# Optimization experiments

Hardware: AMD Instinct MI355X
Metric: run time of the kernel (lower is better)

## Reference

```python
import jax, jax.numpy as jnp
from jax import lax
import numpy as np

# Dims
B_, CIN, COUT, T = 2, 64, 128, 8192
K, NM, N, DCONV, EXP = 5, 2, 16, 4, 2   # kernel, n_mamba, d_state, d_conv, expand
DI = EXP * COUT                          # d_inner = 256
DTR = (COUT + 15) // 16                  # dt_rank = 8
M = NM * 2                               # mamba instances (fwd+bwd per block)


def setup_inputs() -> dict:
    key = jax.random.key(0)
    ks = jax.random.split(key, 8)
    r = lambda k, s, sc=0.02: (jax.random.normal(k, s) * sc).astype(jnp.float32)
    return {
        "x": jax.random.normal(ks[0], (B_, CIN, T), dtype=jnp.float32),
        "conv_w": r(ks[1], (COUT, CIN, K), 0.05),
        "conv_b": jnp.zeros((COUT,), jnp.float32),
        "gn_g": jnp.ones((COUT,), jnp.float32),
        "gn_b": jnp.zeros((COUT,), jnp.float32),
        "prelu_a": jnp.full((1,), 0.25, jnp.float32),
        "ln_g": jnp.ones((NM, COUT), jnp.float32),
        "ln_b": jnp.zeros((NM, COUT), jnp.float32),
        "W_in": r(ks[2], (M, 2 * DI, COUT)),
        "conv1d_w": r(ks[3], (M, DI, 1, DCONV), 0.1),
        "conv1d_b": jnp.zeros((M, DI), jnp.float32),
        "W_xproj": r(ks[4], (M, DTR + 2 * N, DI)),
        "W_dt": r(ks[5], (M, DI, DTR), 0.1),
        "b_dt": jnp.full((M, DI), -4.0, jnp.float32),
        "A_log": jnp.broadcast_to(jnp.log(jnp.arange(1, N + 1, dtype=jnp.float32)), (M, DI, N)).copy(),
        "D_param": jnp.ones((M, DI), jnp.float32),
        "W_out": r(ks[6], (M, COUT, DI)),
    }


def _silu(x):
    return x * jax.nn.sigmoid(x)


def _layernorm(x, g, b, eps=1e-5):
    mu = x.mean(-1, keepdims=True)
    v = ((x - mu) ** 2).mean(-1, keepdims=True)
    return (x - mu) * lax.rsqrt(v + eps) * g + b


def _mamba(h, Wi, cw, cb, Wx, Wd, bd, Alog, Dp, Wo):
    # h: [B, L, d_model] -> [B, L, d_model]. Standard Mamba (S6) block.
    Bb, L, _ = h.shape
    xz = jnp.einsum('bld,ed->ble', h, Wi)               # [B,L,2*DI]
    xp, z = jnp.split(xz, 2, axis=-1)
    xc = jnp.transpose(xp, (0, 2, 1))                   # [B,DI,L]
    xc = lax.conv_general_dilated(xc, cw, (1,), [(DCONV - 1, 0)],
                                  feature_group_count=DI,
                                  dimension_numbers=('NCH', 'OIH', 'NCH')) + cb[None, :, None]
    u = _silu(jnp.transpose(xc, (0, 2, 1)))             # [B,L,DI]
    xdbl = jnp.einsum('bld,ed->ble', u, Wx)             # [B,L,DTR+2N]
    dt, Bm, Cm = jnp.split(xdbl, [DTR, DTR + N], axis=-1)
    delta = jax.nn.softplus(jnp.einsum('blr,dr->bld', dt, Wd) + bd)  # [B,L,DI]
    A = -jnp.exp(Alog)                                  # [DI,N]
    dA = jnp.exp(delta[..., None] * A)                  # [B,L,DI,N]
    dBu = (delta * u)[..., None] * Bm[:, :, None, :]    # [B,L,DI,N]

    def step(hc, inp):
        a, b, c = inp
        hc = a * hc + b                                  # [B,DI,N]
        return hc, jnp.einsum('bdn,bn->bd', hc, c)

    h0 = jnp.zeros((Bb, DI, N), dtype=h.dtype)
    _, ys = lax.scan(step, h0, (jnp.moveaxis(dA, 1, 0), jnp.moveaxis(dBu, 1, 0), jnp.moveaxis(Cm, 1, 0)))
    y = jnp.moveaxis(ys, 0, 1) + u * Dp                 # [B,L,DI]
    y = y * _silu(z)
    return jnp.einsum('ble,de->bld', y, Wo)


def reference(x, conv_w, conv_b, gn_g, gn_b, prelu_a, ln_g, ln_b, W_in,
              conv1d_w, conv1d_b, W_xproj, W_dt, b_dt, A_log, D_param, W_out):
    # Conv1d stride 2, padding K//2: [B,CIN,T] -> [B,COUT,T//2]
    h = lax.conv_general_dilated(x, conv_w, (2,), [(K // 2, K // 2)],
                                 dimension_numbers=('NCH', 'OIH', 'NCH')) + conv_b[None, :, None]
    # GroupNorm(1, COUT): normalize jointly over (C, T)
    mu = h.mean((1, 2), keepdims=True)
    v = ((h - mu) ** 2).mean((1, 2), keepdims=True)
    h = (h - mu) * lax.rsqrt(v + 1e-5) * gn_g[None, :, None] + gn_b[None, :, None]
    h = jnp.where(h >= 0, h, prelu_a[0] * h)            # PReLU (shared scalar)
    h = jnp.transpose(h, (0, 2, 1))                     # [B, L, C]
    for i in range(NM):
        hn = _layernorm(h, ln_g[i], ln_b[i])
        f, bw = 2 * i, 2 * i + 1
        yf = _mamba(hn, W_in[f], conv1d_w[f], conv1d_b[f], W_xproj[f], W_dt[f], b_dt[f], A_log[f], D_param[f], W_out[f])
        hb = jnp.flip(hn, axis=1)
        yb = jnp.flip(_mamba(hb, W_in[bw], conv1d_w[bw], conv1d_b[bw], W_xproj[bw], W_dt[bw], b_dt[bw], A_log[bw], D_param[bw], W_out[bw]), axis=1)
        h = h + yf + yb                                  # bidirectional residual
    return jnp.transpose(h, (0, 2, 1))                   # [B, COUT, T//2]
```

## Files before the change

kernel.cpp:

```cpp
#include <hip/hip_runtime.h>
#include <hip/hip_bf16.h>
#include <math.h>

constexpr int B2   = 2;
constexpr int CIN  = 64;
constexpr int COUT = 128;
constexpr int T    = 8192;
constexpr int L    = 4096;
constexpr int DI   = 256;
constexpr int NST  = 16;
constexpr int DTR  = 8;
constexpr int Q    = 32;
constexpr int NC   = 128;
constexpr int TOK  = B2 * L;

typedef __attribute__((ext_vector_type(8))) short bf16x8s;
typedef __attribute__((ext_vector_type(4))) float f32x4;

__device__ __forceinline__ float sigmoidf_(float x) { return 1.f / (1.f + __expf(-x)); }
__device__ __forceinline__ unsigned short f2bf(float f) {
    unsigned int u = __float_as_uint(f);
    unsigned int r = (u + 0x7FFFu + ((u >> 16) & 1u)) >> 16;
    return (unsigned short)r;
}
__device__ __forceinline__ float bf2f(unsigned short s) {
    return __uint_as_float((unsigned int)s << 16);
}

__global__ __launch_bounds__(256) void prep_all_kernel(
    const float* __restrict__ W_in, const float* __restrict__ W_out,
    const float* __restrict__ cw,
    unsigned short* __restrict__ Winb, unsigned short* __restrict__ Woutb,
    unsigned short* __restrict__ Wrb, float* __restrict__ stats) {
    int idx = blockIdx.x * 256 + threadIdx.x;
    if (blockIdx.x == 0 && threadIdx.x < 4) stats[threadIdx.x] = 0.f;
    if (idx < 262144) {
        Winb[idx] = f2bf(W_in[idx]);
    } else if (idx < 393216) {
        int i = idx - 262144; Woutb[i] = f2bf(W_out[i]);
    } else if (idx < 434176) {
        int i = idx - 393216;
        int co = i / 320, r = i % 320;
        int kp = r >> 6, ci = r & 63;
        Wrb[i] = f2bf(cw[co * 320 + ci * 5 + kp]);
    }
}

__global__ __launch_bounds__(256) void xpose_kernel(
    const float* __restrict__ x, unsigned short* __restrict__ xTb) {
    __shared__ float tile[64][65];
    int b = blockIdx.y, tb = blockIdx.x * 64, tid = threadIdx.x;
    #pragma unroll
    for (int i = 0; i < 16; ++i) {
        int idx = i * 256 + tid; int ci = idx >> 6, tt = idx & 63;
        tile[ci][tt] = x[((size_t)b * CIN + ci) * T + tb + tt];
    }
    __syncthreads();
    #pragma unroll
    for (int i = 0; i < 16; ++i) {
        int idx = i * 256 + tid; int tt = idx >> 6, ci = idx & 63;
        xTb[((size_t)b * T + tb + tt) * 64 + ci] = f2bf(tile[ci][tt]);
    }
}

__global__ __launch_bounds__(256) void conv_mfma_kernel(
    const unsigned short* __restrict__ xTb, const unsigned short* __restrict__ Wrb,
    const float* __restrict__ cb, float* __restrict__ h, float* __restrict__ stats) {
    const int tid = threadIdx.x;
    const int w = tid >> 6, lane = tid & 63, q = lane >> 4, c = lane & 15;
    const int t0g = blockIdx.x * 64;
    const int t0  = t0g + w * 16;
    const int ct0 = blockIdx.y * 64;
    const int b   = t0g >> 12;
    const int l   = (t0 + c) & (L - 1);
    f32x4 acc[4] = {};
    for (int kc = 0; kc < 320; kc += 32) {
        int kp  = kc >> 6;
        int ci0 = (kc & 63) + q * 8;
        int p = 2 * l + kp - 2;
        bf16x8s a = {};
        if (p >= 0 && p < T)
            a = *(const bf16x8s*)&xTb[((size_t)b * T + p) * 64 + ci0];
        #pragma unroll
        for (int i = 0; i < 4; ++i) {
            bf16x8s bb = *(const bf16x8s*)&Wrb[(size_t)(ct0 + i * 16 + c) * 320 + kc + q * 8];
            acc[i] = __builtin_amdgcn_mfma_f32_16x16x32_bf16(a, bb, acc[i], 0, 0, 0);
        }
    }
    float s = 0.f, ss = 0.f;
    #pragma unroll
    for (int i = 0; i < 4; ++i) {
        int cout = ct0 + i * 16 + c;
        float bias = cb[cout];
        #pragma unroll
        for (int r = 0; r < 4; ++r) {
            int tok = t0 + q * 4 + r;
            float v = acc[i][r] + bias;
            h[(size_t)tok * COUT + cout] = v;
            s += v; ss += v * v;
        }
    }
    #pragma unroll
    for (int off = 32; off; off >>= 1) {
        s  += __shfl_down(s,  off, 64);
        ss += __shfl_down(ss, off, 64);
    }
    if (lane == 0) {
        atomicAdd(&stats[b * 2 + 0], s);
        atomicAdd(&stats[b * 2 + 1], ss);
    }
}

__global__ __launch_bounds__(256) void gn_prelu_kernel(
    float* __restrict__ h, const float* __restrict__ gn_g,
    const float* __restrict__ gn_b, const float* __restrict__ prelu_a,
    const float* __restrict__ stats) {
    int i = blockIdx.x * 256 + threadIdx.x;
    size_t base = (size_t)i * 4;
    int b = (base >= (size_t)L * COUT) ? 1 : 0;
    const float n = (float)(L * COUT);
    float mu   = stats[b * 2 + 0] / n;
    float var  = stats[b * 2 + 1] / n - mu * mu;
    float rstd = rsqrtf(var + 1e-5f);
    float a = prelu_a[0];
    float4 v = *(const float4*)&h[base];
    int c = (int)(base % COUT);
    float4 g  = *(const float4*)&gn_g[c];
    float4 bb = *(const float4*)&gn_b[c];
    v.x = (v.x - mu) * rstd * g.x + bb.x; v.x = v.x >= 0.f ? v.x : a * v.x;
    v.y = (v.y - mu) * rstd * g.y + bb.y; v.y = v.y >= 0.f ? v.y : a * v.y;
    v.z = (v.z - mu) * rstd * g.z + bb.z; v.z = v.z >= 0.f ? v.z : a * v.z;
    v.w = (v.w - mu) * rstd * g.w + bb.w; v.w = v.w >= 0.f ? v.w : a * v.w;
    *(float4*)&h[base] = v;
}

__global__ __launch_bounds__(256) void ln_kernel(
    const float* __restrict__ h, unsigned short* __restrict__ hnb,
    const float* __restrict__ g, const float* __restrict__ bta) {
    int wave = threadIdx.x >> 6, lane = threadIdx.x & 63;
    int t = blockIdx.x * 4 + wave;
    const float* row = h + (size_t)t * COUT;
    float2 v = *(const float2*)&row[lane * 2];
    float s = v.x + v.y, ss = v.x * v.x + v.y * v.y;
    #pragma unroll
    for (int off = 32; off; off >>= 1) {
        s  += __shfl_xor(s,  off, 64);
        ss += __shfl_xor(ss, off, 64);
    }
    float mu = s * (1.f / 128.f);
    float var = ss * (1.f / 128.f) - mu * mu;
    float rstd = rsqrtf(var + 1e-5f);
    float2 gg = *(const float2*)&g[lane * 2];
    float2 bb = *(const float2*)&bta[lane * 2];
    ushort2 o;
    o.x = f2bf((v.x - mu) * rstd * gg.x + bb.x);
    o.y = f2bf((v.y - mu) * rstd * gg.y + bb.y);
    *(ushort2*)&hnb[(size_t)t * COUT + lane * 2] = o;
}

__global__ __launch_bounds__(256) void inproj_mfma_kernel(
    const unsigned short* __restrict__ hnb, const unsigned short* __restrict__ Winb,
    float* __restrict__ xp0, unsigned short* __restrict__ zb0,
    float* __restrict__ xp1, unsigned short* __restrict__ zb1, int layer) {
    const int tid = threadIdx.x;
    const int w = tid >> 6, lane = tid & 63, q = lane >> 4, c = lane & 15;
    const int t0 = blockIdx.x * 64 + w * 16;
    const int nBase = blockIdx.y * 64;
    const int inst = nBase >> 9;
    const int e0 = nBase & 511;
    const unsigned short* Wb = Winb + (size_t)(layer * 2 + inst) * 512 * 128;
    f32x4 acc[4] = {};
    for (int kc = 0; kc < 128; kc += 32) {
        bf16x8s a = *(const bf16x8s*)&hnb[(size_t)(t0 + c) * 128 + kc + q * 8];
        #pragma unroll
        for (int i = 0; i < 4; ++i) {
            bf16x8s bb = *(const bf16x8s*)&Wb[(size_t)(e0 + i * 16 + c) * 128 + kc + q * 8];
            acc[i] = __builtin_amdgcn_mfma_f32_16x16x32_bf16(a, bb, acc[i], 0, 0, 0);
        }
    }
    #pragma unroll
    for (int i = 0; i < 4; ++i) {
        int e = e0 + i * 16 + c;
        bool isz = (e >= 256);
        int eo = e & 255;
        #pragma unroll
        for (int r = 0; r < 4; ++r) {
            int tok = t0 + q * 4 + r;
            float v = acc[i][r];
            if (isz) {
                float sv = v * sigmoidf_(v);
                (inst ? zb1 : zb0)[(size_t)tok * DI + eo] = f2bf(sv);
            } else {
                (inst ? xp1 : xp0)[(size_t)tok * DI + eo] = v;
            }
        }
    }
}

__global__ __launch_bounds__(256) void dwconv_kernel(
    const float* __restrict__ xp0, const float* __restrict__ xp1,
    const float* __restrict__ cw, const float* __restrict__ cbias,
    float* __restrict__ u0, float* __restrict__ u1, int layer) {
    int flat = blockIdx.x * 256 + threadIdx.x;
    int dq   = flat & 63;
    int l    = (flat >> 6) & (L - 1);
    int b    = (flat >> 18) & 1;
    int inst = flat >> 19;
    const float* xp = inst ? xp1 : xp0;
    float* u = inst ? u1 : u0;
    int m = layer * 2 + inst;
    int d0 = dq * 4;
    float4 w0 = *(const float4*)&cw[(size_t)(m * DI + d0 + 0) * 4];
    float4 w1 = *(const float4*)&cw[(size_t)(m * DI + d0 + 1) * 4];
    float4 w2 = *(const float4*)&cw[(size_t)(m * DI + d0 + 2) * 4];
    float4 w3 = *(const float4*)&cw[(size_t)(m * DI + d0 + 3) * 4];
    float4 acc = *(const float4*)&cbias[m * DI + d0];
    size_t base = ((size_t)b * L) * DI + d0;
    if (inst == 0) {
        if (l >= 3) { float4 v = *(const float4*)&xp[base + (size_t)(l - 3) * DI];
            acc.x = fmaf(w0.x, v.x, acc.x); acc.y = fmaf(w1.x, v.y, acc.y);
            acc.z = fmaf(w2.x, v.z, acc.z); acc.w = fmaf(w3.x, v.w, acc.w); }
        if (l >= 2) { float4 v = *(const float4*)&xp[base + (size_t)(l - 2) * DI];
            acc.x = fmaf(w0.y, v.x, acc.x); acc.y = fmaf(w1.y, v.y, acc.y);
            acc.z = fmaf(w2.y, v.z, acc.z); acc.w = fmaf(w3.y, v.w, acc.w); }
        if (l >= 1) { float4 v = *(const float4*)&xp[base + (size_t)(l - 1) * DI];
            acc.x = fmaf(w0.z, v.x, acc.x); acc.y = fmaf(w1.z, v.y, acc.y);
            acc.z = fmaf(w2.z, v.z, acc.z); acc.w = fmaf(w3.z, v.w, acc.w); }
        { float4 v = *(const float4*)&xp[base + (size_t)l * DI];
            acc.x = fmaf(w0.w, v.x, acc.x); acc.y = fmaf(w1.w, v.y, acc.y);
            acc.z = fmaf(w2.w, v.z, acc.z); acc.w = fmaf(w3.w, v.w, acc.w); }
    } else {
        { float4 v = *(const float4*)&xp[base + (size_t)l * DI];
            acc.x = fmaf(w0.w, v.x, acc.x); acc.y = fmaf(w1.w, v.y, acc.y);
            acc.z = fmaf(w2.w, v.z, acc.z); acc.w = fmaf(w3.w, v.w, acc.w); }
        if (l + 1 < L) { float4 v = *(const float4*)&xp[base + (size_t)(l + 1) * DI];
            acc.x = fmaf(w0.z, v.x, acc.x); acc.y = fmaf(w1.z, v.y, acc.y);
            acc.z = fmaf(w2.z, v.z, acc.z); acc.w = fmaf(w3.z, v.w, acc.w); }
        if (l + 2 < L) { float4 v = *(const float4*)&xp[base + (size_t)(l + 2) * DI];
            acc.x = fmaf(w0.y, v.x, acc.x); acc.y = fmaf(w1.y, v.y, acc.y);
            acc.z = fmaf(w2.y, v.z, acc.z); acc.w = fmaf(w3.y, v.w, acc.w); }
        if (l + 3 < L) { float4 v = *(const float4*)&xp[base + (size_t)(l + 3) * DI];
            acc.x = fmaf(w0.x, v.x, acc.x); acc.y = fmaf(w1.x, v.y, acc.y);
            acc.z = fmaf(w2.x, v.z, acc.z); acc.w = fmaf(w3.x, v.w, acc.w); }
    }
    acc.x *= sigmoidf_(acc.x); acc.y *= sigmoidf_(acc.y);
    acc.z *= sigmoidf_(acc.z); acc.w *= sigmoidf_(acc.w);
    *(float4*)&u[base + (size_t)l * DI] = acc;
}

__global__ __launch_bounds__(256) void xproj_kernel(
    const float* __restrict__ u0, const float* __restrict__ u1,
    const float* __restrict__ Wx, const float* __restrict__ Wdt,
    const float* __restrict__ bdt,
    float* __restrict__ dl0, float* __restrict__ dl1,
    float* __restrict__ Bm0, float* __restrict__ Bm1,
    float* __restrict__ Cm0, float* __restrict__ Cm1, int layer) {
    __shared__ float Ws[40 * 132];
    __shared__ float As[128 * 33];
    __shared__ float xd[32 * 9];
    const int tid   = threadIdx.x;
    const int tBase = blockIdx.x * 32;
    const int inst  = blockIdx.y;
    const int m     = layer * 2 + inst;
    const float* u  = inst ? u1 : u0;
    const float* Wm = Wx + (size_t)m * 40 * 256;
    const int t  = tid & 31;
    const int eq = tid >> 5;
    float acc[5] = {};
    for (int kc = 0; kc < 256; kc += 128) {
        __syncthreads();
        #pragma unroll
        for (int i = 0; i < 5; ++i) {
            int idx = i * 256 + tid;
            int e = idx >> 5, kq = idx & 31;
            float4 w4 = *(const float4*)&Wm[(size_t)e * 256 + kc + kq * 4];
            float* dstw = &Ws[e * 132 + kq * 4];
            dstw[0] = w4.x; dstw[1] = w4.y; dstw[2] = w4.z; dstw[3] = w4.w;
        }
        #pragma unroll
        for (int i = 0; i < 4; ++i) {
            int flat = i * 256 + tid;
            int tt = flat >> 5, kq = flat & 31;
            float4 v = *(const float4*)&u[(size_t)(tBase + tt) * DI + kc + kq * 4];
            As[(kq * 4 + 0) * 33 + tt] = v.x;
            As[(kq * 4 + 1) * 33 + tt] = v.y;
            As[(kq * 4 + 2) * 33 + tt] = v.z;
            As[(kq * 4 + 3) * 33 + tt] = v.w;
        }
        __syncthreads();
        #pragma unroll 4
        for (int kk = 0; kk < 128; ++kk) {
            float a = As[kk * 33 + t];
            acc[0] = fmaf(a, Ws[(eq     ) * 132 + kk], acc[0]);
            acc[1] = fmaf(a, Ws[(eq +  8) * 132 + kk], acc[1]);
            acc[2] = fmaf(a, Ws[(eq + 16) * 132 + kk], acc[2]);
            acc[3] = fmaf(a, Ws[(eq + 24) * 132 + kk], acc[3]);
            acc[4] = fmaf(a, Ws[(eq + 32) * 132 + kk], acc[4]);
        }
    }
    {
        int tok = tBase + t;
        float* Bm = inst ? Bm1 : Bm0;
        float* Cm = inst ? Cm1 : Cm0;
        xd[t * 9 + eq] = acc[0];
        Bm[(size_t)tok * NST + eq]     = acc[1];
        Bm[(size_t)tok * NST + 8 + eq] = acc[2];
        Cm[(size_t)tok * NST + eq]     = acc[3];
        Cm[(size_t)tok * NST + 8 + eq] = acc[4];
    }
    __syncthreads();
    {
        int d = tid;
        float wr[8];
        #pragma unroll
        for (int r = 0; r < 8; ++r) wr[r] = Wdt[((size_t)m * DI + d) * DTR + r];
        float bb = bdt[m * DI + d];
        float* dl = inst ? dl1 : dl0;
        #pragma unroll 4
        for (int tt = 0; tt < 32; ++tt) {
            float a2 = bb;
            #pragma unroll
            for (int r = 0; r < 8; ++r) a2 = fmaf(xd[tt * 9 + r], wr[r], a2);
            float sp = fmaxf(a2, 0.f) + __logf(1.f + __expf(-fabsf(a2)));
            dl[(size_t)(tBase + tt) * DI + d] = sp;
        }
    }
}

__global__ __launch_bounds__(256) void scan1_kernel(
    const float* __restrict__ dl0, const float* __restrict__ dl1,
    const float* __restrict__ u0,  const float* __restrict__ u1,
    const float* __restrict__ Bm0, const float* __restrict__ Bm1,
    const float* __restrict__ A_log,
    float* __restrict__ hend, float* __restrict__ dsumb, int layer) {
    const int tid = threadIdx.x;
    const int nq = tid & 3, dlane = tid >> 2;
    const int chunk = blockIdx.x & (NC - 1), dtile = blockIdx.x >> 7;
    const int b = blockIdx.y, inst = blockIdx.z;
    const int m = layer * 2 + inst, dir = inst;
    const int d = dtile * 64 + dlane;
    const float* dl = inst ? dl1 : dl0;
    const float* u  = inst ? u1  : u0;
    const float* Bm = inst ? Bm1 : Bm0;
    float4 av = *(const float4*)&A_log[((size_t)m * DI + d) * NST + nq * 4];
    const float a0 = -expf(av.x), a1 = -expf(av.y), a2 = -expf(av.z), a3 = -expf(av.w);
    const int s0 = chunk * Q;
    const int l0 = dir ? (L - 1 - s0) : s0;
    const int stp = dir ? -1 : 1;
    long iDU = ((long)(b * L + l0)) * DI + d;
    int  iB  = ((b * L + l0) << 4) + nq * 4;
    const long sDU = (long)stp * DI;
    const int  sB  = stp * NST;
    float h0 = 0.f, h1 = 0.f, h2 = 0.f, h3 = 0.f, dsum = 0.f;
    #pragma unroll 4
    for (int t = 0; t < Q; ++t) {
        float dlt = dl[iDU], uu = u[iDU];
        float4 bm = *(const float4*)&Bm[iB];
        float du = dlt * uu;
        h0 = fmaf(__expf(dlt * a0), h0, du * bm.x);
        h1 = fmaf(__expf(dlt * a1), h1, du * bm.y);
        h2 = fmaf(__expf(dlt * a2), h2, du * bm.z);
        h3 = fmaf(__expf(dlt * a3), h3, du * bm.w);
        dsum += dlt;
        iDU += sDU; iB += sB;
    }
    size_t oh = (((size_t)(inst * 2 + b) * DI + d) * NC + chunk) * NST + nq * 4;
    *(float4*)&hend[oh] = make_float4(h0, h1, h2, h3);
    if (nq == 0) dsumb[((size_t)(inst * 2 + b) * NC + chunk) * DI + d] = dsum;
}

__global__ __launch_bounds__(256) void combine_kernel(
    float* __restrict__ hend, const float* __restrict__ dsumb,
    const float* __restrict__ A_log, int layer) {
    int flat = blockIdx.x * 256 + threadIdx.x;
    int n = flat & 15;
    int d = (flat >> 4) & 255;
    int b = (flat >> 12) & 1;
    int inst = flat >> 13;
    int m = layer * 2 + inst;
    float a = -expf(A_log[((size_t)m * DI + d) * NST + n]);
    size_t baseE = (((size_t)(inst * 2 + b) * DI + d) * NC) * NST + n;
    size_t baseD = ((size_t)(inst * 2 + b) * NC) * DI + d;
    float hc = 0.f;
    #pragma unroll 4
    for (int c = 0; c < NC; ++c) {
        float tmp = hend[baseE + (size_t)c * NST];
        hend[baseE + (size_t)c * NST] = hc;
        float ds = dsumb[baseD + (size_t)c * DI];
        hc = fmaf(__expf(a * ds), hc, tmp);
    }
}

__global__ __launch_bounds__(256) void scan2_kernel(
    const float* __restrict__ dl0, const float* __restrict__ dl1,
    const float* __restrict__ u0,  const float* __restrict__ u1,
    const float* __restrict__ Bm0, const float* __restrict__ Bm1,
    const float* __restrict__ Cm0, const float* __restrict__ Cm1,
    unsigned short* __restrict__ zb0, unsigned short* __restrict__ zb1,
    const float* __restrict__ hin, const float* __restrict__ A_log,
    const float* __restrict__ Dp, int layer) {
    const int tid = threadIdx.x;
    const int nq = tid & 3, dlane = tid >> 2;
    const int chunk = blockIdx.x & (NC - 1), dtile = blockIdx.x >> 7;
    const int b = blockIdx.y, inst = blockIdx.z;
    const int m = layer * 2 + inst, dir = inst;
    const int d = dtile * 64 + dlane;
    const float* dl = inst ? dl1 : dl0;
    const float* u  = inst ? u1  : u0;
    const float* Bm = inst ? Bm1 : Bm0;
    const float* Cm = inst ? Cm1 : Cm0;
    unsigned short* zs = inst ? zb1 : zb0;
    float4 av = *(const float4*)&A_log[((size_t)m * DI + d) * NST + nq * 4];
    const float a0 = -expf(av.x), a1 = -expf(av.y), a2 = -expf(av.z), a3 = -expf(av.w);
    const float dpar = Dp[m * DI + d];
    const int s0 = chunk * Q;
    const int l0 = dir ? (L - 1 - s0) : s0;
    const int stp = dir ? -1 : 1;
    long iDU = ((long)(b * L + l0)) * DI + d;
    int  iB  = ((b * L + l0) << 4) + nq * 4;
    const long sDU = (long)stp * DI;
    const int  sB  = stp * NST;
    float4 hv = *(const float4*)&hin[(((size_t)(inst * 2 + b) * DI + d) * NC + chunk) * NST + nq * 4];
    float h0 = hv.x, h1 = hv.y, h2 = hv.z, h3 = hv.w;
    #pragma unroll 4
    for (int t = 0; t < Q; ++t) {
        float dlt = dl[iDU], uu = u[iDU];
        float4 bm = *(const float4*)&Bm[iB];
        float4 cm = *(const float4*)&Cm[iB];
        float du = dlt * uu;
        h0 = fmaf(__expf(dlt * a0), h0, du * bm.x);
        h1 = fmaf(__expf(dlt * a1), h1, du * bm.y);
        h2 = fmaf(__expf(dlt * a2), h2, du * bm.z);
        h3 = fmaf(__expf(dlt * a3), h3, du * bm.w);
        float yp = h0 * cm.x + h1 * cm.y + h2 * cm.z + h3 * cm.w;
        yp += __shfl_xor(yp, 1, 4);
        yp += __shfl_xor(yp, 2, 4);
        if (nq == 0) {
            float zv = bf2f(zs[iDU]);
            zs[iDU] = f2bf(fmaf(uu, dpar, yp) * zv);
        }
        iDU += sDU; iB += sB;
    }
}

__global__ __launch_bounds__(256) void outproj_mfma_kernel(
    const unsigned short* __restrict__ ygb0, const unsigned short* __restrict__ ygb1,
    const unsigned short* __restrict__ Woutb, float* __restrict__ h, int layer) {
    const int tid = threadIdx.x;
    const int w = tid >> 6, lane = tid & 63, q = lane >> 4, c = lane & 15;
    const int t0 = blockIdx.x * 64 + w * 16;
    const int ct0 = blockIdx.y * 32;
    f32x4 acc[2] = {};
    #pragma unroll
    for (int inst = 0; inst < 2; ++inst) {
        const unsigned short* yg = inst ? ygb1 : ygb0;
        const unsigned short* Wb = Woutb + (size_t)(layer * 2 + inst) * COUT * DI;
        for (int kc = 0; kc < 256; kc += 32) {
            bf16x8s a = *(const bf16x8s*)&yg[(size_t)(t0 + c) * DI + kc + q * 8];
            #pragma unroll
            for (int i = 0; i < 2; ++i) {
                bf16x8s bb = *(const bf16x8s*)&Wb[(size_t)(ct0 + i * 16 + c) * DI + kc + q * 8];
                acc[i] = __builtin_amdgcn_mfma_f32_16x16x32_bf16(a, bb, acc[i], 0, 0, 0);
            }
        }
    }
    #pragma unroll
    for (int i = 0; i < 2; ++i) {
        int cout = ct0 + i * 16 + c;
        #pragma unroll
        for (int r = 0; r < 4; ++r) {
            int tok = t0 + q * 4 + r;
            h[(size_t)tok * COUT + cout] += acc[i][r];
        }
    }
}

__global__ __launch_bounds__(256) void transpose_kernel(
    const float* __restrict__ h, float* __restrict__ out) {
    __shared__ float tile[32][33];
    int lt0 = blockIdx.x * 32, ct0 = blockIdx.y * 32, b = blockIdx.z;
    int c = threadIdx.x & 31, r = threadIdx.x >> 5;
    #pragma unroll
    for (int j = 0; j < 4; ++j) {
        int ll = r + 8 * j;
        tile[ll][c] = h[((size_t)b * L + lt0 + ll) * COUT + ct0 + c];
    }
    __syncthreads();
    #pragma unroll
    for (int j = 0; j < 4; ++j) {
        int cc = r + 8 * j;
        out[((size_t)b * COUT + ct0 + cc) * L + lt0 + c] = tile[c][cc];
    }
}

extern "C" void kernel_launch(void* const* d_in, const int* in_sizes, int n_in,
                              void* d_out, int out_size, void* d_ws, size_t ws_size,
                              hipStream_t stream) {
    const float* x        = (const float*)d_in[0];
    const float* conv_w   = (const float*)d_in[1];
    const float* conv_b   = (const float*)d_in[2];
    const float* gn_g     = (const float*)d_in[3];
    const float* gn_b     = (const float*)d_in[4];
    const float* prelu_a  = (const float*)d_in[5];
    const float* ln_g     = (const float*)d_in[6];
    const float* ln_b     = (const float*)d_in[7];
    const float* W_in     = (const float*)d_in[8];
    const float* conv1d_w = (const float*)d_in[9];
    const float* conv1d_b = (const float*)d_in[10];
    const float* W_xproj  = (const float*)d_in[11];
    const float* W_dt     = (const float*)d_in[12];
    const float* b_dt     = (const float*)d_in[13];
    const float* A_log    = (const float*)d_in[14];
    const float* D_param  = (const float*)d_in[15];
    const float* W_out    = (const float*)d_in[16];

    float* ws = (float*)d_ws;
    float* h     = ws;
    float* xp0   = ws + 1048576;
    float* xp1   = ws + 3145728;
    unsigned short* zb0 = (unsigned short*)(ws + 5242880);
    unsigned short* zb1 = (unsigned short*)(ws + 6291456);
    float* u0    = ws + 7340032;
    float* u1    = ws + 9437184;
    float* dl0   = ws + 11534336;
    float* dl1   = ws + 13631488;
    float* Bm0   = ws + 15728640;
    float* Bm1   = ws + 15859712;
    float* Cm0   = ws + 15990784;
    float* Cm1   = ws + 16121856;
    float* hend  = ws + 16252928;
    float* dsumb = ws + 18350080;
    unsigned short* Winb  = (unsigned short*)(ws + 18481152);
    unsigned short* Wrb   = (unsigned short*)(ws + 18612224);
    unsigned short* Woutb = (unsigned short*)(ws + 18632704);
    float* stats = ws + 18698240;
    unsigned short* hnb = (unsigned short*)hend;
    unsigned short* xTb = zb0;

    prep_all_kernel<<<1696, 256, 0, stream>>>(W_in, W_out, conv_w, Winb, Woutb, Wrb, stats);
    xpose_kernel<<<dim3(T / 64, B2), 256, 0, stream>>>(x, xTb);
    conv_mfma_kernel<<<dim3(TOK / 64, COUT / 64), 256, 0, stream>>>(xTb, Wrb, conv_b, h, stats);
    gn_prelu_kernel<<<(TOK * COUT / 4) / 256, 256, 0, stream>>>(h, gn_g, gn_b, prelu_a, stats);

    for (int layer = 0; layer < 2; ++layer) {
        ln_kernel<<<TOK / 4, 256, 0, stream>>>(h, hnb, ln_g + layer * COUT, ln_b + layer * COUT);
        inproj_mfma_kernel<<<dim3(TOK / 64, 16), 256, 0, stream>>>(hnb, Winb, xp0, zb0, xp1, zb1, layer);
        dwconv_kernel<<<4096, 256, 0, stream>>>(xp0, xp1, conv1d_w, conv1d_b, u0, u1, layer);
        xproj_kernel<<<dim3(TOK / 32, 2), 256, 0, stream>>>(u0, u1, W_xproj, W_dt, b_dt,
                                                            dl0, dl1, Bm0, Bm1, Cm0, Cm1, layer);
        scan1_kernel<<<dim3(NC * 4, B2, 2), 256, 0, stream>>>(dl0, dl1, u0, u1, Bm0, Bm1,
                                                              A_log, hend, dsumb, layer);
        combine_kernel<<<64, 256, 0, stream>>>(hend, dsumb, A_log, layer);
        scan2_kernel<<<dim3(NC * 4, B2, 2), 256, 0, stream>>>(dl0, dl1, u0, u1, Bm0, Bm1, Cm0, Cm1,
                                                              zb0, zb1, hend, A_log, D_param, layer);
        outproj_mfma_kernel<<<dim3(TOK / 64, 4), 256, 0, stream>>>(zb0, zb1, Woutb, h, layer);
    }
    transpose_kernel<<<dim3(L / 32, COUT / 32, B2), 256, 0, stream>>>(h, (float*)d_out);
}
```

Baseline: 393.0 us.

## Fuse depthwise conv into in-projection and GroupNorm into first LayerNorm

The in-projection kernel now keeps the x-branch output tile, plus a 16-token halo recomputed by one wave, in shared memory. It applies the causal or anti-causal depthwise conv and SiLU there and writes u directly, which removes the fp32 xp round trip to global memory and one launch per layer. Separately, GroupNorm+PReLU is fused with the layer-0 LayerNorm so h is read once. The cost is redundant halo MFMA work and a serialized extra pass on wave 0 in x-branch blocks, plus an LDS stage and barrier.

```diff
diff --git a/kernel.cpp b/kernel.cpp
--- a/kernel.cpp
+++ b/kernel.cpp
@@ -111,27 +111,41 @@
     }
 }
 
-__global__ __launch_bounds__(256) void gn_prelu_kernel(
+__global__ __launch_bounds__(256) void gn_ln_kernel(
     float* __restrict__ h, const float* __restrict__ gn_g,
     const float* __restrict__ gn_b, const float* __restrict__ prelu_a,
-    const float* __restrict__ stats) {
-    int i = blockIdx.x * 256 + threadIdx.x;
-    size_t base = (size_t)i * 4;
-    int b = (base >= (size_t)L * COUT) ? 1 : 0;
+    const float* __restrict__ stats, unsigned short* __restrict__ hnb,
+    const float* __restrict__ lng, const float* __restrict__ lnb) {
+    int wave = threadIdx.x >> 6, lane = threadIdx.x & 63;
+    int t = blockIdx.x * 4 + wave;
+    int b = t >> 12;
     const float n = (float)(L * COUT);
     float mu   = stats[b * 2 + 0] / n;
     float var  = stats[b * 2 + 1] / n - mu * mu;
     float rstd = rsqrtf(var + 1e-5f);
     float a = prelu_a[0];
-    float4 v = *(const float4*)&h[base];
-    int c = (int)(base % COUT);
-    float4 g  = *(const float4*)&gn_g[c];
-    float4 bb = *(const float4*)&gn_b[c];
+    float* row = h + (size_t)t * COUT;
+    float2 v  = *(const float2*)&row[lane * 2];
+    float2 g  = *(const float2*)&gn_g[lane * 2];
+    float2 bb = *(const float2*)&gn_b[lane * 2];
     v.x = (v.x - mu) * rstd * g.x + bb.x; v.x = v.x >= 0.f ? v.x : a * v.x;
     v.y = (v.y - mu) * rstd * g.y + bb.y; v.y = v.y >= 0.f ? v.y : a * v.y;
-    v.z = (v.z - mu) * rstd * g.z + bb.z; v.z = v.z >= 0.f ? v.z : a * v.z;
-    v.w = (v.w - mu) * rstd * g.w + bb.w; v.w = v.w >= 0.f ? v.w : a * v.w;
-    *(float4*)&h[base] = v;
+    *(float2*)&row[lane * 2] = v;
+    float s = v.x + v.y, ss = v.x * v.x + v.y * v.y;
+    #pragma unroll
+    for (int off = 32; off; off >>= 1) {
+        s  += __shfl_xor(s,  off, 64);
+        ss += __shfl_xor(ss, off, 64);
+    }
+    float mu2 = s * (1.f / 128.f);
+    float var2 = ss * (1.f / 128.f) - mu2 * mu2;
+    float rstd2 = rsqrtf(var2 + 1e-5f);
+    float2 gg = *(const float2*)&lng[lane * 2];
+    float2 lb = *(const float2*)&lnb[lane * 2];
+    ushort2 o;
+    o.x = f2bf((v.x - mu2) * rstd2 * gg.x + lb.x);
+    o.y = f2bf((v.y - mu2) * rstd2 * gg.y + lb.y);
+    *(ushort2*)&hnb[(size_t)t * COUT + lane * 2] = o;
 }
 
 __global__ __launch_bounds__(256) void ln_kernel(
@@ -158,94 +172,98 @@
     *(ushort2*)&hnb[(size_t)t * COUT + lane * 2] = o;
 }
 
-__global__ __launch_bounds__(256) void inproj_mfma_kernel(
+__global__ __launch_bounds__(256) void inproj_dw_kernel(
     const unsigned short* __restrict__ hnb, const unsigned short* __restrict__ Winb,
-    float* __restrict__ xp0, unsigned short* __restrict__ zb0,
-    float* __restrict__ xp1, unsigned short* __restrict__ zb1, int layer) {
+    const float* __restrict__ cw, const float* __restrict__ cbias,
+    float* __restrict__ u0, float* __restrict__ u1,
+    unsigned short* __restrict__ zb0, unsigned short* __restrict__ zb1, int layer) {
+    __shared__ float xs[80 * 68];
     const int tid = threadIdx.x;
     const int w = tid >> 6, lane = tid & 63, q = lane >> 4, c = lane & 15;
-    const int t0 = blockIdx.x * 64 + w * 16;
+    const int tBase = blockIdx.x * 64;
     const int nBase = blockIdx.y * 64;
     const int inst = nBase >> 9;
     const int e0 = nBase & 511;
-    const unsigned short* Wb = Winb + (size_t)(layer * 2 + inst) * 512 * 128;
-    f32x4 acc[4] = {};
-    for (int kc = 0; kc < 128; kc += 32) {
-        bf16x8s a = *(const bf16x8s*)&hnb[(size_t)(t0 + c) * 128 + kc + q * 8];
+    const int m = layer * 2 + inst;
+    const unsigned short* Wb = Winb + (size_t)m * 512 * 128;
+
+    if (e0 >= 256) {
+        const int t0 = tBase + w * 16;
+        f32x4 acc[4] = {};
+        for (int kc = 0; kc < 128; kc += 32) {
+            bf16x8s a = *(const bf16x8s*)&hnb[(size_t)(t0 + c) * 128 + kc + q * 8];
+            #pragma unroll
+            for (int i = 0; i < 4; ++i) {
+                bf16x8s bb = *(const bf16x8s*)&Wb[(size_t)(e0 + i * 16 + c) * 128 + kc + q * 8];
+                acc[i] = __builtin_amdgcn_mfma_f32_16x16x32_bf16(a, bb, acc[i], 0, 0, 0);
+            }
+        }
+        unsigned short* zb = inst ? zb1 : zb0;
         #pragma unroll
         for (int i = 0; i < 4; ++i) {
-            bf16x8s bb = *(const bf16x8s*)&Wb[(size_t)(e0 + i * 16 + c) * 128 + kc + q * 8];
-            acc[i] = __builtin_amdgcn_mfma_f32_16x16x32_bf16(a, bb, acc[i], 0, 0, 0);
-        }
-    }
-    #pragma unroll
-    for (int i = 0; i < 4; ++i) {
-        int e = e0 + i * 16 + c;
-        bool isz = (e >= 256);
-        int eo = e & 255;
-        #pragma unroll
-        for (int r = 0; r < 4; ++r) {
-            int tok = t0 + q * 4 + r;
-            float v = acc[i][r];
-            if (isz) {
-                float sv = v * sigmoidf_(v);
-                (inst ? zb1 : zb0)[(size_t)tok * DI + eo] = f2bf(sv);
-            } else {
-                (inst ? xp1 : xp0)[(size_t)tok * DI + eo] = v;
+            int eo = (e0 + i * 16 + c) & 255;
+            #pragma unroll
+            for (int r = 0; r < 4; ++r) {
+                int tok = t0 + q * 4 + r;
+                float v = acc[i][r];
+                zb[(size_t)tok * DI + eo] = f2bf(v * sigmoidf_(v));
             }
         }
-    }
-}
-
-__global__ __launch_bounds__(256) void dwconv_kernel(
-    const float* __restrict__ xp0, const float* __restrict__ xp1,
-    const float* __restrict__ cw, const float* __restrict__ cbias,
-    float* __restrict__ u0, float* __restrict__ u1, int layer) {
-    int flat = blockIdx.x * 256 + threadIdx.x;
-    int dq   = flat & 63;
-    int l    = (flat >> 6) & (L - 1);
-    int b    = (flat >> 18) & 1;
-    int inst = flat >> 19;
-    const float* xp = inst ? xp1 : xp0;
-    float* u = inst ? u1 : u0;
-    int m = layer * 2 + inst;
-    int d0 = dq * 4;
+        return;
+    }
+    const int winT0 = (inst == 0) ? (tBase - 16) : tBase;
+    for (int pass = 0; pass < 2; ++pass) {
+        if (pass == 1 && w != 0) break;
+        int slot = (pass == 0) ? (w + (inst == 0 ? 1 : 0))
+                               : ((inst == 0) ? 0 : 4);
+        int tokA = winT0 + slot * 16 + c;
+        tokA = tokA < 0 ? 0 : (tokA > TOK - 1 ? TOK - 1 : tokA);
+        f32x4 acc[4] = {};
+        for (int kc = 0; kc < 128; kc += 32) {
+            bf16x8s a = *(const bf16x8s*)&hnb[(size_t)tokA * 128 + kc + q * 8];
+            #pragma unroll
+            for (int i = 0; i < 4; ++i) {
+                bf16x8s bb = *(const bf16x8s*)&Wb[(size_t)(e0 + i * 16 + c) * 128 + kc + q * 8];
+                acc[i] = __builtin_amdgcn_mfma_f32_16x16x32_bf16(a, bb, acc[i], 0, 0, 0);
+            }
+        }
+        #pragma unroll
+        for (int i = 0; i < 4; ++i)
+            #pragma unroll
+            for (int r = 0; r < 4; ++r)
+                xs[(slot * 16 + q * 4 + r) * 68 + i * 16 + c] = acc[i][r];
+    }
+    __syncthreads();
+    const int l0base = tBase & (L - 1);
+    const int ch4 = tid & 15;
+    const int d0 = e0 + ch4 * 4;
     float4 w0 = *(const float4*)&cw[(size_t)(m * DI + d0 + 0) * 4];
     float4 w1 = *(const float4*)&cw[(size_t)(m * DI + d0 + 1) * 4];
     float4 w2 = *(const float4*)&cw[(size_t)(m * DI + d0 + 2) * 4];
     float4 w3 = *(const float4*)&cw[(size_t)(m * DI + d0 + 3) * 4];
-    float4 acc = *(const float4*)&cbias[m * DI + d0];
-    size_t base = ((size_t)b * L) * DI + d0;
-    if (inst == 0) {
-        if (l >= 3) { float4 v = *(const float4*)&xp[base + (size_t)(l - 3) * DI];
-            acc.x = fmaf(w0.x, v.x, acc.x); acc.y = fmaf(w1.x, v.y, acc.y);
-            acc.z = fmaf(w2.x, v.z, acc.z); acc.w = fmaf(w3.x, v.w, acc.w); }
-        if (l >= 2) { float4 v = *(const float4*)&xp[base + (size_t)(l - 2) * DI];
-            acc.x = fmaf(w0.y, v.x, acc.x); acc.y = fmaf(w1.y, v.y, acc.y);
-            acc.z = fmaf(w2.y, v.z, acc.z); acc.w = fmaf(w3.y, v.w, acc.w); }
-        if (l >= 1) { float4 v = *(const float4*)&xp[base + (size_t)(l - 1) * DI];
-            acc.x = fmaf(w0.z, v.x, acc.x); acc.y = fmaf(w1.z, v.y, acc.y);
-            acc.z = fmaf(w2.z, v.z, acc.z); acc.w = fmaf(w3.z, v.w, acc.w); }
-        { float4 v = *(const float4*)&xp[base + (size_t)l * DI];
-            acc.x = fmaf(w0.w, v.x, acc.x); acc.y = fmaf(w1.w, v.y, acc.y);
-            acc.z = fmaf(w2.w, v.z, acc.z); acc.w = fmaf(w3.w, v.w, acc.w); }
-    } else {
-        { float4 v = *(const float4*)&xp[base + (size_t)l * DI];
-            acc.x = fmaf(w0.w, v.x, acc.x); acc.y = fmaf(w1.w, v.y, acc.y);
-            acc.z = fmaf(w2.w, v.z, acc.z); acc.w = fmaf(w3.w, v.w, acc.w); }
-        if (l + 1 < L) { float4 v = *(const float4*)&xp[base + (size_t)(l + 1) * DI];
-            acc.x = fmaf(w0.z, v.x, acc.x); acc.y = fmaf(w1.z, v.y, acc.y);
-            acc.z = fmaf(w2.z, v.z, acc.z); acc.w = fmaf(w3.z, v.w, acc.w); }
-        if (l + 2 < L) { float4 v = *(const float4*)&xp[base + (size_t)(l + 2) * DI];
-            acc.x = fmaf(w0.y, v.x, acc.x); acc.y = fmaf(w1.y, v.y, acc.y);
-            acc.z = fmaf(w2.y, v.z, acc.z); acc.w = fmaf(w3.y, v.w, acc.w); }
-        if (l + 3 < L) { float4 v = *(const float4*)&xp[base + (size_t)(l + 3) * DI];
-            acc.x = fmaf(w0.x, v.x, acc.x); acc.y = fmaf(w1.x, v.y, acc.y);
-            acc.z = fmaf(w2.x, v.z, acc.z); acc.w = fmaf(w3.x, v.w, acc.w); }
-    }
-    acc.x *= sigmoidf_(acc.x); acc.y *= sigmoidf_(acc.y);
-    acc.z *= sigmoidf_(acc.z); acc.w *= sigmoidf_(acc.w);
-    *(float4*)&u[base + (size_t)l * DI] = acc;
+    float4 bias4 = *(const float4*)&cbias[m * DI + d0];
+    float* ud = inst ? u1 : u0;
+    #pragma unroll
+    for (int p = 0; p < 4; ++p) {
+        int j = p * 16 + (tid >> 4);
+        float4 acc = bias4;
+        #pragma unroll
+        for (int k = 0; k < 4; ++k) {
+            bool valid = (inst == 0) ? (l0base + j - 3 + k >= 0)
+                                     : (l0base + j + 3 - k < L);
+            if (valid) {
+                int wj = (inst == 0) ? (j + 13 + k) : (j + 3 - k);
+                float4 v = *(const float4*)&xs[wj * 68 + ch4 * 4];
+                float wk0 = ((const float*)&w0)[k], wk1 = ((const float*)&w1)[k];
+                float wk2 = ((const float*)&w2)[k], wk3 = ((const float*)&w3)[k];
+                acc.x = fmaf(wk0, v.x, acc.x); acc.y = fmaf(wk1, v.y, acc.y);
+                acc.z = fmaf(wk2, v.z, acc.z); acc.w = fmaf(wk3, v.w, acc.w);
+            }
+        }
+        acc.x *= sigmoidf_(acc.x); acc.y *= sigmoidf_(acc.y);
+        acc.z *= sigmoidf_(acc.z); acc.w *= sigmoidf_(acc.w);
+        *(float4*)&ud[(size_t)(tBase + j) * DI + d0] = acc;
+    }
 }
 
 __global__ __launch_bounds__(256) void xproj_kernel(
@@ -516,8 +534,6 @@
 
     float* ws = (float*)d_ws;
     float* h     = ws;
-    float* xp0   = ws + 1048576;
-    float* xp1   = ws + 3145728;
     unsigned short* zb0 = (unsigned short*)(ws + 5242880);
     unsigned short* zb1 = (unsigned short*)(ws + 6291456);
     float* u0    = ws + 7340032;
@@ -540,12 +556,13 @@
     prep_all_kernel<<<1696, 256, 0, stream>>>(W_in, W_out, conv_w, Winb, Woutb, Wrb, stats);
     xpose_kernel<<<dim3(T / 64, B2), 256, 0, stream>>>(x, xTb);
     conv_mfma_kernel<<<dim3(TOK / 64, COUT / 64), 256, 0, stream>>>(xTb, Wrb, conv_b, h, stats);
-    gn_prelu_kernel<<<(TOK * COUT / 4) / 256, 256, 0, stream>>>(h, gn_g, gn_b, prelu_a, stats);
+    gn_ln_kernel<<<TOK / 4, 256, 0, stream>>>(h, gn_g, gn_b, prelu_a, stats, hnb, ln_g, ln_b);
 
     for (int layer = 0; layer < 2; ++layer) {
-        ln_kernel<<<TOK / 4, 256, 0, stream>>>(h, hnb, ln_g + layer * COUT, ln_b + layer * COUT);
-        inproj_mfma_kernel<<<dim3(TOK / 64, 16), 256, 0, stream>>>(hnb, Winb, xp0, zb0, xp1, zb1, layer);
-        dwconv_kernel<<<4096, 256, 0, stream>>>(xp0, xp1, conv1d_w, conv1d_b, u0, u1, layer);
+        if (layer == 1)
+            ln_kernel<<<TOK / 4, 256, 0, stream>>>(h, hnb, ln_g + COUT, ln_b + COUT);
+        inproj_dw_kernel<<<dim3(TOK / 64, 16), 256, 0, stream>>>(hnb, Winb, conv1d_w, conv1d_b,
+                                                                 u0, u1, zb0, zb1, layer);
         xproj_kernel<<<dim3(TOK / 32, 2), 256, 0, stream>>>(u0, u1, W_xproj, W_dt, b_dt,
                                                             dl0, dl1, Bm0, Bm1, Cm0, Cm1, layer);
         scan1_kernel<<<dim3(NC * 4, B2, 2), 256, 0, stream>>>(dl0, dl1, u0, u1, Bm0, Bm1,
```

Result: faster. 378.6 us (median of 2 runs) (-3.7%).
